# Kernel optimization log

Measured on AMD Instinct MI355X. Metric: run time of the kernel, lower is better.

The kernel has to match this reference:

```python
import jax, jax.numpy as jnp
import numpy as np

NEG_INF = -1e9  # large negative for masking (avoid NaN rows under -inf with fully masked rows)
LEAKY_SLOPE = 0.2

def setup_inputs() -> dict:
    key = jax.random.key(0)
    k1, k2, k3, k4, k5 = jax.random.split(key, 5)
    N, in_dim, out_dim = 8192, 512, 64
    x = jax.random.normal(k1, (N, in_dim), dtype=jnp.float32)
    adj = jax.random.randint(k2, (N, N), 0, 2, dtype=jnp.int32)
    W = jax.random.normal(k3, (out_dim, in_dim), dtype=jnp.float32) * (1.0 / np.sqrt(in_dim))
    a_src = jax.random.normal(k4, (out_dim,), dtype=jnp.float32)
    a_dst = jax.random.normal(k5, (out_dim,), dtype=jnp.float32)
    return {"x": x, "adj": adj, "W": W, "a_src": a_src, "a_dst": a_dst}

def reference(x, adj, W, a_src, a_dst):
    # Linear projection: Wh[n, d]
    Wh = x @ W.T
    # Additive GAT attention: e[i, j] = LeakyReLU(a_src . Wh_i + a_dst . Wh_j)
    s = Wh @ a_src  # [N]
    d = Wh @ a_dst  # [N]
    e = jax.nn.leaky_relu(s[:, None] + d[None, :], negative_slope=LEAKY_SLOPE)  # [N, N]
    e = jnp.where(adj > 0, e, NEG_INF)
    alpha = jax.nn.softmax(e, axis=1)  # [N, N]
    # Dropout on alpha is identity in eval/reference mode.
    h_prime = alpha @ Wh  # [N, out_dim]
    return h_prime
```

## Files before the change

kernel.cpp:

```cpp
#include <hip/hip_runtime.h>

#define GN 8192
#define IN_DIM 512
#define ODIM 64
#define SLOPE 0.2f
#define PB 128
#define CB 2048
#define JSPLIT 16
#define JCH (GN / JSPLIT)

typedef __attribute__((ext_vector_type(4))) float  f32x4;
typedef __attribute__((ext_vector_type(4))) int    i32x4;
typedef __attribute__((ext_vector_type(8))) short  bf16x8;
typedef __attribute__((ext_vector_type(4))) unsigned short u16x4;

static __device__ __forceinline__ float bf2f(unsigned short u) {
    return __uint_as_float(((unsigned)u) << 16);
}
static __device__ __forceinline__ unsigned short f2bf(float f) {
    union { float f; unsigned u; } c; c.f = f;
    unsigned b = c.u;
    return (unsigned short)((b + 0x7fffu + ((b >> 16) & 1u)) >> 16);
}

static __device__ __forceinline__ bf16x8 load8(const void* p, size_t off, int f32) {
    if (f32) {
        f32x4 lo = *(const f32x4*)((const float*)p + off);
        f32x4 hi = *(const f32x4*)((const float*)p + off + 4);
        bf16x8 r;
        #pragma unroll
        for (int q = 0; q < 4; ++q) {
            r[q]     = (short)f2bf(lo[q]);
            r[4 + q] = (short)f2bf(hi[q]);
        }
        return r;
    }
    return *(const bf16x8*)((const ushort*)p + off);
}

extern "C" __global__ __launch_bounds__(256)
void gat_prep(const void* __restrict__ x_, const void* __restrict__ W_,
              const void* __restrict__ as_, const void* __restrict__ ad_,
              const int* __restrict__ adj, unsigned long long* __restrict__ bits64,
              ushort* __restrict__ WhT, float* __restrict__ s_arr,
              float* __restrict__ d_arr, int* __restrict__ dmax_bits,
              int* __restrict__ dflag)
{
    const int wave = threadIdx.x >> 6;
    const int lane = threadIdx.x & 63;

    if (blockIdx.x >= PB) {
        const int wid = (blockIdx.x - PB) * 4 + wave;
        const size_t stride = (size_t)CB * 4 * 256;
        #pragma unroll 2
        for (int it = 0; it < 32; ++it) {
            const size_t base = (size_t)wid * 256 + (size_t)it * stride;
            int a0 = adj[base +   0 + lane];
            int a1 = adj[base +  64 + lane];
            int a2 = adj[base + 128 + lane];
            int a3 = adj[base + 192 + lane];
            unsigned long long b0 = __ballot(a0 > 0);
            unsigned long long b1 = __ballot(a1 > 0);
            unsigned long long b2 = __ballot(a2 > 0);
            unsigned long long b3 = __ballot(a3 > 0);
            if (lane == 0) {
                ulonglong2* p = (ulonglong2*)(bits64 + base / 64);
                p[0] = make_ulonglong2(b0, b1);
                p[1] = make_ulonglong2(b2, b3);
            }
        }
        return;
    }

    unsigned xw = ((const unsigned*)x_)[lane];
    unsigned ef = (xw >> 23) & 0xffu;
    unsigned long long vt = __ballot(ef > 60u && ef < 180u);
    const int f32 = (__popcll(vt) >= 32) ? 1 : 0;
    if (blockIdx.x == 0 && threadIdx.x == 0) *dflag = f32;

    const int quad = lane >> 4;
    const int lq   = lane & 15;
    const int i0   = blockIdx.x * 64 + wave * 16;

    f32x4 acc[4] = {{0,0,0,0},{0,0,0,0},{0,0,0,0},{0,0,0,0}};
    const size_t arow = (size_t)(i0 + lq) * IN_DIM;
    #pragma unroll 2
    for (int k0 = 0; k0 < IN_DIM; k0 += 32) {
        const int kk = k0 + quad * 8;
        bf16x8 a  = load8(x_, arow + kk, f32);
        bf16x8 b0 = load8(W_, (size_t)( 0 + lq) * IN_DIM + kk, f32);
        bf16x8 b1 = load8(W_, (size_t)(16 + lq) * IN_DIM + kk, f32);
        bf16x8 b2 = load8(W_, (size_t)(32 + lq) * IN_DIM + kk, f32);
        bf16x8 b3 = load8(W_, (size_t)(48 + lq) * IN_DIM + kk, f32);
        acc[0] = __builtin_amdgcn_mfma_f32_16x16x32_bf16(a, b0, acc[0], 0, 0, 0);
        acc[1] = __builtin_amdgcn_mfma_f32_16x16x32_bf16(a, b1, acc[1], 0, 0, 0);
        acc[2] = __builtin_amdgcn_mfma_f32_16x16x32_bf16(a, b2, acc[2], 0, 0, 0);
        acc[3] = __builtin_amdgcn_mfma_f32_16x16x32_bf16(a, b3, acc[3], 0, 0, 0);
    }
    float av_s[4], av_d[4];
    #pragma unroll
    for (int t = 0; t < 4; ++t) {
        const int n = t * 16 + lq;
        av_s[t] = f32 ? ((const float*)as_)[n] : bf2f(((const ushort*)as_)[n]);
        av_d[t] = f32 ? ((const float*)ad_)[n] : bf2f(((const ushort*)ad_)[n]);
    }
    #pragma unroll
    for (int t = 0; t < 4; ++t) {
        u16x4 pk;
        #pragma unroll
        for (int r = 0; r < 4; ++r) pk[r] = f2bf(acc[t][r]);
        *(u16x4*)(WhT + (size_t)(t * 16 + lq) * GN + i0 + quad * 4) = pk;
    }
    float ps[4], pd[4];
    #pragma unroll
    for (int r = 0; r < 4; ++r) {
        float s = 0.f, d = 0.f;
        #pragma unroll
        for (int t = 0; t < 4; ++t) {
            s = fmaf(acc[t][r], av_s[t], s);
            d = fmaf(acc[t][r], av_d[t], d);
        }
        #pragma unroll
        for (int off = 1; off < 16; off <<= 1) {
            s += __shfl_xor(s, off);
            d += __shfl_xor(d, off);
        }
        ps[r] = s; pd[r] = d;
    }
    if (lq == 0) {
        float dmx = -1e30f;
        #pragma unroll
        for (int r = 0; r < 4; ++r) {
            s_arr[i0 + quad * 4 + r] = ps[r];
            d_arr[i0 + quad * 4 + r] = pd[r];
            dmx = fmaxf(dmx, pd[r]);
        }
        if (dmx > 0.f) atomicMax(dmax_bits, __float_as_int(dmx));
    }
}

extern "C" __global__ __launch_bounds__(256, 4)
void gat_attn(const unsigned* __restrict__ bits32, const ushort* __restrict__ WhT,
              const float* __restrict__ s_arr, const float* __restrict__ d_arr,
              const int* __restrict__ dmax_bits,
              float* __restrict__ accum, float* __restrict__ lsum)
{
    const int ib   = blockIdx.x & 127;
    const int js   = blockIdx.x >> 7;
    const int wave = threadIdx.x >> 6;
    const int lane = threadIdx.x & 63;
    const int quad = lane >> 4;
    const int lq   = lane & 15;
    const int i = ib * 64 + wave * 16 + lq;
    const float dmax = __int_as_float(*dmax_bits);
    const float si = s_arr[i];
    const float tb = si + dmax;
    const float mi = fmaxf(tb, SLOPE * tb);
    const int jbase = js * JCH;
    f32x4 acc0 = {0,0,0,0}, acc1 = {0,0,0,0}, acc2 = {0,0,0,0}, acc3 = {0,0,0,0};
    float lacc = 0.f;
    const unsigned* bitrow = bits32 + (size_t)i * (GN / 32) + js * (JCH / 32);

    #pragma unroll 1
    for (int it4 = 0; it4 < JCH / 128; ++it4) {
        i32x4 bw = *(const i32x4*)(bitrow + it4 * 4);
        #pragma unroll
        for (int sub = 0; sub < 4; ++sub) {
            const int it = it4 * 4 + sub;
            const int j0 = jbase + it * 32 + quad * 8;
            const unsigned m8 = (((unsigned)bw[sub]) >> (quad * 8)) & 0xffu;
            f32x4 dv0 = *(const f32x4*)(d_arr + j0);
            f32x4 dv1 = *(const f32x4*)(d_arr + j0 + 4);
            bf16x8 b0 = *(const bf16x8*)(WhT + (size_t)( 0 + lq) * GN + j0);
            bf16x8 b1 = *(const bf16x8*)(WhT + (size_t)(16 + lq) * GN + j0);
            bf16x8 b2 = *(const bf16x8*)(WhT + (size_t)(32 + lq) * GN + j0);
            bf16x8 b3 = *(const bf16x8*)(WhT + (size_t)(48 + lq) * GN + j0);
            float w[8];
            #pragma unroll
            for (int q = 0; q < 4; ++q) {
                float e0 = si + dv0[q];
                e0 = fmaxf(e0, SLOPE * e0);
                float v0 = __expf(e0 - mi);
                w[q] = ((m8 >> q) & 1u) ? v0 : 0.f;
                float e1 = si + dv1[q];
                e1 = fmaxf(e1, SLOPE * e1);
                float v1 = __expf(e1 - mi);
                w[4 + q] = ((m8 >> (4 + q)) & 1u) ? v1 : 0.f;
            }
            bf16x8 af;
            #pragma unroll
            for (int q = 0; q < 8; ++q) {
                unsigned short wb = f2bf(w[q]);
                af[q] = (short)wb;
                lacc += bf2f(wb);
            }
            acc0 = __builtin_amdgcn_mfma_f32_16x16x32_bf16(af, b0, acc0, 0, 0, 0);
            acc1 = __builtin_amdgcn_mfma_f32_16x16x32_bf16(af, b1, acc1, 0, 0, 0);
            acc2 = __builtin_amdgcn_mfma_f32_16x16x32_bf16(af, b2, acc2, 0, 0, 0);
            acc3 = __builtin_amdgcn_mfma_f32_16x16x32_bf16(af, b3, acc3, 0, 0, 0);
        }
    }
    lacc += __shfl_xor(lacc, 16);
    lacc += __shfl_xor(lacc, 32);
    if (quad == 0) atomicAdd(&lsum[i], lacc);
    const int orow = ib * 64 + wave * 16 + quad * 4;
    #pragma unroll
    for (int r = 0; r < 4; ++r) {
        atomicAdd(&accum[(size_t)(orow + r) * ODIM +  0 + lq], acc0[r]);
        atomicAdd(&accum[(size_t)(orow + r) * ODIM + 16 + lq], acc1[r]);
        atomicAdd(&accum[(size_t)(orow + r) * ODIM + 32 + lq], acc2[r]);
        atomicAdd(&accum[(size_t)(orow + r) * ODIM + 48 + lq], acc3[r]);
    }
}

extern "C" __global__ __launch_bounds__(256)
void gat_final(const float* __restrict__ accum, const float* __restrict__ lsum,
               const int* __restrict__ flag, void* __restrict__ out)
{
    const int idx = blockIdx.x * 256 + threadIdx.x;
    const float v = accum[idx] / lsum[idx >> 6];
    if (*flag) ((float*)out)[idx] = v;
    else       ((ushort*)out)[idx] = f2bf(v);
}

extern "C" void kernel_launch(void* const* d_in, const int* in_sizes, int n_in,
                              void* d_out, int out_size, void* d_ws, size_t ws_size,
                              hipStream_t stream)
{
    const void* x     = d_in[0];
    const int*  adj   = (const int*)d_in[1];
    const void* W     = d_in[2];
    const void* a_src = d_in[3];
    const void* a_dst = d_in[4];

    char* ws = (char*)d_ws;
    size_t off = 0;
    float* accum = (float*)(ws + off);  off += (size_t)GN * ODIM * 4;
    float* lsum  = (float*)(ws + off);  off += (size_t)GN * 4;
    int* dmax_bits = (int*)(ws + off);  off += 128;
    size_t zero_bytes = off;
    int* dflag = (int*)(ws + off);      off += 128;
    float* s_arr = (float*)(ws + off);  off += (size_t)GN * 4;
    float* d_arr = (float*)(ws + off);  off += (size_t)GN * 4;
    ushort* WhT  = (ushort*)(ws + off); off += (size_t)ODIM * GN * 2;
    unsigned long long* bits = (unsigned long long*)(ws + off);
    off += (size_t)GN * GN / 8;

    hipMemsetAsync(ws, 0, zero_bytes, stream);
    gat_prep<<<PB + CB, 256, 0, stream>>>(x, W, a_src, a_dst, adj, bits,
                                          WhT, s_arr, d_arr, dmax_bits, dflag);
    gat_attn<<<128 * JSPLIT, 256, 0, stream>>>((const unsigned*)bits, WhT,
                                               s_arr, d_arr, dmax_bits, accum, lsum);
    gat_final<<<GN * ODIM / 256, 256, 0, stream>>>(accum, lsum, dflag, d_out);
}
```

Before: 457.5 us.

## Fuse adjacency bitmask packing into attention kernel via shared memory

Removes the separate adjacency-to-bitmask pass in the prep kernel. Each attention block now reads its own 64x512 tile of the int32 adjacency matrix, packs it into bytes in LDS, and consumes the mask from there. This drops the global bitmask write and re-read and lets the projection run as a small standalone kernel. The row-sum of weights is also moved from scalar accumulation onto an extra MFMA against a ones vector, at the cost of one more MFMA per step and removal of the occupancy hint.

```diff
diff --git a/kernel.cpp b/kernel.cpp
--- a/kernel.cpp
+++ b/kernel.cpp
@@ -4,10 +4,9 @@
 #define IN_DIM 512
 #define ODIM 64
 #define SLOPE 0.2f
-#define PB 128
-#define CB 2048
 #define JSPLIT 16
 #define JCH (GN / JSPLIT)
+#define LSTRIDE 68
 
 typedef __attribute__((ext_vector_type(4))) float  f32x4;
 typedef __attribute__((ext_vector_type(4))) int    i32x4;
@@ -39,39 +38,14 @@
 }
 
 extern "C" __global__ __launch_bounds__(256)
-void gat_prep(const void* __restrict__ x_, const void* __restrict__ W_,
+void gat_proj(const void* __restrict__ x_, const void* __restrict__ W_,
               const void* __restrict__ as_, const void* __restrict__ ad_,
-              const int* __restrict__ adj, unsigned long long* __restrict__ bits64,
               ushort* __restrict__ WhT, float* __restrict__ s_arr,
               float* __restrict__ d_arr, int* __restrict__ dmax_bits,
               int* __restrict__ dflag)
 {
     const int wave = threadIdx.x >> 6;
     const int lane = threadIdx.x & 63;
-
-    if (blockIdx.x >= PB) {
-        const int wid = (blockIdx.x - PB) * 4 + wave;
-        const size_t stride = (size_t)CB * 4 * 256;
-        #pragma unroll 2
-        for (int it = 0; it < 32; ++it) {
-            const size_t base = (size_t)wid * 256 + (size_t)it * stride;
-            int a0 = adj[base +   0 + lane];
-            int a1 = adj[base +  64 + lane];
-            int a2 = adj[base + 128 + lane];
-            int a3 = adj[base + 192 + lane];
-            unsigned long long b0 = __ballot(a0 > 0);
-            unsigned long long b1 = __ballot(a1 > 0);
-            unsigned long long b2 = __ballot(a2 > 0);
-            unsigned long long b3 = __ballot(a3 > 0);
-            if (lane == 0) {
-                ulonglong2* p = (ulonglong2*)(bits64 + base / 64);
-                p[0] = make_ulonglong2(b0, b1);
-                p[1] = make_ulonglong2(b2, b3);
-            }
-        }
-        return;
-    }
-
     unsigned xw = ((const unsigned*)x_)[lane];
     unsigned ef = (xw >> 23) & 0xffu;
     unsigned long long vt = __ballot(ef > 60u && ef < 180u);
@@ -139,71 +113,87 @@
     }
 }
 
-extern "C" __global__ __launch_bounds__(256, 4)
-void gat_attn(const unsigned* __restrict__ bits32, const ushort* __restrict__ WhT,
+extern "C" __global__ __launch_bounds__(256)
+void gat_attn(const int* __restrict__ adj, const ushort* __restrict__ WhT,
               const float* __restrict__ s_arr, const float* __restrict__ d_arr,
               const int* __restrict__ dmax_bits,
               float* __restrict__ accum, float* __restrict__ lsum)
 {
+    __shared__ unsigned char mb[64 * LSTRIDE];
     const int ib   = blockIdx.x & 127;
     const int js   = blockIdx.x >> 7;
     const int wave = threadIdx.x >> 6;
     const int lane = threadIdx.x & 63;
     const int quad = lane >> 4;
     const int lq   = lane & 15;
-    const int i = ib * 64 + wave * 16 + lq;
+    const int i0   = ib * 64;
+    const int jbase = js * JCH;
+
+    #pragma unroll 4
+    for (int s = 0; s < 16; ++s) {
+        const int r = s * 4 + wave;
+        const int* row = adj + (size_t)(i0 + r) * GN + jbase;
+        i32x4 a0 = *(const i32x4*)(row + lane * 8);
+        i32x4 a1 = *(const i32x4*)(row + lane * 8 + 4);
+        unsigned byte = 0;
+        #pragma unroll
+        for (int q = 0; q < 4; ++q) {
+            byte |= (a0[q] > 0 ? 1u : 0u) << q;
+            byte |= (a1[q] > 0 ? 1u : 0u) << (4 + q);
+        }
+        mb[r * LSTRIDE + lane] = (unsigned char)byte;
+    }
+    __syncthreads();
+
+    const int li = wave * 16 + lq;
+    const int i  = i0 + li;
     const float dmax = __int_as_float(*dmax_bits);
     const float si = s_arr[i];
     const float tb = si + dmax;
     const float mi = fmaxf(tb, SLOPE * tb);
-    const int jbase = js * JCH;
     f32x4 acc0 = {0,0,0,0}, acc1 = {0,0,0,0}, acc2 = {0,0,0,0}, acc3 = {0,0,0,0};
-    float lacc = 0.f;
-    const unsigned* bitrow = bits32 + (size_t)i * (GN / 32) + js * (JCH / 32);
-
-    #pragma unroll 1
-    for (int it4 = 0; it4 < JCH / 128; ++it4) {
-        i32x4 bw = *(const i32x4*)(bitrow + it4 * 4);
-        #pragma unroll
-        for (int sub = 0; sub < 4; ++sub) {
-            const int it = it4 * 4 + sub;
-            const int j0 = jbase + it * 32 + quad * 8;
-            const unsigned m8 = (((unsigned)bw[sub]) >> (quad * 8)) & 0xffu;
-            f32x4 dv0 = *(const f32x4*)(d_arr + j0);
-            f32x4 dv1 = *(const f32x4*)(d_arr + j0 + 4);
-            bf16x8 b0 = *(const bf16x8*)(WhT + (size_t)( 0 + lq) * GN + j0);
-            bf16x8 b1 = *(const bf16x8*)(WhT + (size_t)(16 + lq) * GN + j0);
-            bf16x8 b2 = *(const bf16x8*)(WhT + (size_t)(32 + lq) * GN + j0);
-            bf16x8 b3 = *(const bf16x8*)(WhT + (size_t)(48 + lq) * GN + j0);
-            float w[8];
-            #pragma unroll
-            for (int q = 0; q < 4; ++q) {
-                float e0 = si + dv0[q];
-                e0 = fmaxf(e0, SLOPE * e0);
-                float v0 = __expf(e0 - mi);
-                w[q] = ((m8 >> q) & 1u) ? v0 : 0.f;
-                float e1 = si + dv1[q];
-                e1 = fmaxf(e1, SLOPE * e1);
-                float v1 = __expf(e1 - mi);
-                w[4 + q] = ((m8 >> (4 + q)) & 1u) ? v1 : 0.f;
-            }
-            bf16x8 af;
-            #pragma unroll
-            for (int q = 0; q < 8; ++q) {
-                unsigned short wb = f2bf(w[q]);
-                af[q] = (short)wb;
-                lacc += bf2f(wb);
-            }
-            acc0 = __builtin_amdgcn_mfma_f32_16x16x32_bf16(af, b0, acc0, 0, 0, 0);
-            acc1 = __builtin_amdgcn_mfma_f32_16x16x32_bf16(af, b1, acc1, 0, 0, 0);
-            acc2 = __builtin_amdgcn_mfma_f32_16x16x32_bf16(af, b2, acc2, 0, 0, 0);
-            acc3 = __builtin_amdgcn_mfma_f32_16x16x32_bf16(af, b3, acc3, 0, 0, 0);
-        }
-    }
-    lacc += __shfl_xor(lacc, 16);
-    lacc += __shfl_xor(lacc, 32);
-    if (quad == 0) atomicAdd(&lsum[i], lacc);
-    const int orow = ib * 64 + wave * 16 + quad * 4;
+    f32x4 acc4 = {0,0,0,0};
+    bf16x8 ones;
+    #pragma unroll
+    for (int q = 0; q < 8; ++q) ones[q] = (short)0x3F80;
+
+    #pragma unroll 2
+    for (int it = 0; it < JCH / 32; ++it) {
+        const int j0 = jbase + it * 32 + quad * 8;
+        unsigned bw = *(const unsigned*)(mb + li * LSTRIDE + it * 4);
+        const unsigned m8 = (bw >> (quad * 8)) & 0xffu;
+        f32x4 dv0 = *(const f32x4*)(d_arr + j0);
+        f32x4 dv1 = *(const f32x4*)(d_arr + j0 + 4);
+        bf16x8 b0 = *(const bf16x8*)(WhT + (size_t)( 0 + lq) * GN + j0);
+        bf16x8 b1 = *(const bf16x8*)(WhT + (size_t)(16 + lq) * GN + j0);
+        bf16x8 b2 = *(const bf16x8*)(WhT + (size_t)(32 + lq) * GN + j0);
+        bf16x8 b3 = *(const bf16x8*)(WhT + (size_t)(48 + lq) * GN + j0);
+        float w[8];
+        #pragma unroll
+        for (int q = 0; q < 4; ++q) {
+            float e0 = si + dv0[q];
+            e0 = fmaxf(e0, SLOPE * e0);
+            float v0 = __expf(e0 - mi);
+            w[q] = ((m8 >> q) & 1u) ? v0 : 0.f;
+            float e1 = si + dv1[q];
+            e1 = fmaxf(e1, SLOPE * e1);
+            float v1 = __expf(e1 - mi);
+            w[4 + q] = ((m8 >> (4 + q)) & 1u) ? v1 : 0.f;
+        }
+        bf16x8 af;
+        #pragma unroll
+        for (int q = 0; q < 8; ++q) af[q] = (short)f2bf(w[q]);
+        acc0 = __builtin_amdgcn_mfma_f32_16x16x32_bf16(af, b0, acc0, 0, 0, 0);
+        acc1 = __builtin_amdgcn_mfma_f32_16x16x32_bf16(af, b1, acc1, 0, 0, 0);
+        acc2 = __builtin_amdgcn_mfma_f32_16x16x32_bf16(af, b2, acc2, 0, 0, 0);
+        acc3 = __builtin_amdgcn_mfma_f32_16x16x32_bf16(af, b3, acc3, 0, 0, 0);
+        acc4 = __builtin_amdgcn_mfma_f32_16x16x32_bf16(af, ones, acc4, 0, 0, 0);
+    }
+    const int orow = i0 + wave * 16 + quad * 4;
+    if (lq == 0) {
+        #pragma unroll
+        for (int r = 0; r < 4; ++r) atomicAdd(&lsum[orow + r], acc4[r]);
+    }
     #pragma unroll
     for (int r = 0; r < 4; ++r) {
         atomicAdd(&accum[(size_t)(orow + r) * ODIM +  0 + lq], acc0[r]);
@@ -243,13 +233,11 @@
     float* s_arr = (float*)(ws + off);  off += (size_t)GN * 4;
     float* d_arr = (float*)(ws + off);  off += (size_t)GN * 4;
     ushort* WhT  = (ushort*)(ws + off); off += (size_t)ODIM * GN * 2;
-    unsigned long long* bits = (unsigned long long*)(ws + off);
-    off += (size_t)GN * GN / 8;
 
     hipMemsetAsync(ws, 0, zero_bytes, stream);
-    gat_prep<<<PB + CB, 256, 0, stream>>>(x, W, a_src, a_dst, adj, bits,
+    gat_proj<<<GN / 64, 256, 0, stream>>>(x, W, a_src, a_dst,
                                           WhT, s_arr, d_arr, dmax_bits, dflag);
-    gat_attn<<<128 * JSPLIT, 256, 0, stream>>>((const unsigned*)bits, WhT,
-                                               s_arr, d_arr, dmax_bits, accum, lsum);
+    gat_attn<<<128 * JSPLIT, 256, 0, stream>>>(adj, WhT, s_arr, d_arr,
+                                               dmax_bits, accum, lsum);
     gat_final<<<GN * ODIM / 256, 256, 0, stream>>>(accum, lsum, dflag, d_out);
 }
```

Result: no change. 463.6 us (+1.3%).
